# Optimization experiments

Hardware: AMD Instinct MI355X
Metric: run time of the kernel (lower is better)

Reference implementation:

```python
import jax, jax.numpy as jnp
import numpy as np

N_NODES = 100000
N_EDGES = 1600000
N_CRYS = 2000
NODE_F = 64
EDGE_F = 41
N_CONV = 3
H_F = 128
EPS = 1e-5


def _seg_mean(v, idx, n):
    s = jax.ops.segment_sum(v, idx, num_segments=n)
    c = jax.ops.segment_sum(jnp.ones((v.shape[0], 1), v.dtype), idx, num_segments=n)
    return s / jnp.maximum(c, 1.0)


def _bn(x, g, b):
    # training-mode batch norm over dim 0, biased variance (torch semantics)
    m = x.mean(axis=0)
    v = x.var(axis=0)
    return (x - m) * jax.lax.rsqrt(v + EPS) * g + b


def setup_inputs() -> dict:
    key = jax.random.key(0)
    ks = jax.random.split(key, 16)
    inp = {}
    inp['node_fea'] = jax.random.randint(ks[0], (N_NODES,), 0, 101)
    inp['edge_fea'] = jax.random.normal(ks[1], (N_EDGES, EDGE_F), dtype=jnp.float32)
    inp['idx1'] = jax.random.randint(ks[2], (N_EDGES,), 0, N_NODES)
    inp['idx2'] = jax.random.randint(ks[3], (N_EDGES,), 0, N_NODES)
    inp['idx3'] = jnp.sort(jax.random.randint(ks[4], (N_NODES,), 0, N_CRYS))
    # parameters
    din = 2 * NODE_F + EDGE_F
    sc = 1.0 / np.sqrt(din)
    inp['emb'] = jax.random.normal(ks[5], (101, NODE_F), dtype=jnp.float32)
    inp['Wf'] = jax.random.uniform(ks[6], (N_CONV, din, 2 * NODE_F), jnp.float32, -sc, sc)
    inp['bf'] = jax.random.uniform(ks[7], (N_CONV, 2 * NODE_F), jnp.float32, -sc, sc)
    inp['g1'] = jnp.ones((N_CONV, 2 * NODE_F), jnp.float32)
    inp['be1'] = jnp.zeros((N_CONV, 2 * NODE_F), jnp.float32)
    inp['g2'] = jnp.ones((N_CONV, NODE_F), jnp.float32)
    inp['be2'] = jnp.zeros((N_CONV, NODE_F), jnp.float32)
    sc2 = 1.0 / np.sqrt(NODE_F)
    inp['Wc'] = jax.random.uniform(ks[8], (NODE_F, H_F), jnp.float32, -sc2, sc2)
    inp['bc'] = jax.random.uniform(ks[9], (H_F,), jnp.float32, -sc2, sc2)
    sc3 = 1.0 / np.sqrt(H_F)
    inp['Wo'] = jax.random.uniform(ks[10], (H_F, 2), jnp.float32, -sc3, sc3)
    inp['bo'] = jax.random.uniform(ks[11], (2,), jnp.float32, -sc3, sc3)
    return inp


def reference(node_fea, edge_fea, idx1, idx2, idx3, emb, Wf, bf, g1, be1, g2, be2, Wc, bc, Wo, bo):
    x = emb[node_fea]                                   # [N, 64]
    for l in range(N_CONV):
        z12 = jnp.concatenate([x[idx1], x[idx2], edge_fea], axis=1)   # [E, 169]
        z12 = _bn(z12 @ Wf[l] + bf[l], g1[l], be1[l])   # [E, 128]
        gate, conv = jnp.split(z12, 2, axis=1)
        msg = jax.nn.sigmoid(gate) * jax.nn.softplus(conv)
        node_new = _bn(_seg_mean(msg, idx1, N_NODES), g2[l], be2[l])
        x = jax.nn.softplus(x + node_new)
    crys = _seg_mean(x, idx3, N_CRYS)                   # [C, 64]
    crys = jax.nn.softplus(crys @ Wc + bc)              # [C, 128]
    return crys @ Wo + bo                               # [C, 2]
```

## Files before the change

### kernel.cpp

```cpp
#include <hip/hip_runtime.h>
#include <hip/hip_bf16.h>


#define NN 100000
#define NE 1600000
#define NC 2000
#define KPAD 176
#define EFW 48
#define EPSB 1e-5f
#define NCH 1000
#define CH 100

typedef _Float16 f16;
typedef _Float16 half8 __attribute__((ext_vector_type(8)));
typedef _Float16 half2v __attribute__((ext_vector_type(2)));
typedef float f32x16 __attribute__((ext_vector_type(16)));

__device__ __forceinline__ f32x16 zero16() {
    f32x16 v;
#pragma unroll
    for (int i = 0; i < 16; i++) v[i] = 0.f;
    return v;
}
__device__ __forceinline__ float fsoftplus(float x) {
    return fmaxf(x, 0.f) + __logf(1.f + __expf(-fabsf(x)));
}
__device__ __forceinline__ float fsigmoid(float x) {
    return __fdividef(1.f, 1.f + __expf(-x));
}

__global__ void k_prep_x(const int* __restrict__ nf, const float* __restrict__ emb,
                         float* __restrict__ xf, f16* __restrict__ x16) {
    for (int idx = blockIdx.x * blockDim.x + threadIdx.x; idx < NN * 64;
         idx += gridDim.x * blockDim.x) {
        int n = idx >> 6, k = idx & 63;
        float v = emb[nf[n] * 64 + k];
        xf[idx] = v;
        x16[idx] = (f16)v;
    }
}

__global__ void k_deg(const int* __restrict__ idx1, const int* __restrict__ idx3,
                      int* deg1, float* cnt3) {
    for (int i = blockIdx.x * blockDim.x + threadIdx.x; i < NE;
         i += gridDim.x * blockDim.x) {
        atomicAdd(&deg1[idx1[i]], 1);
        if (i < NN) atomicAdd(&cnt3[idx3[i]], 1.f);
    }
}

__global__ void k_scan_a(const int* __restrict__ deg, int* __restrict__ csum) {
    int t = blockIdx.x * blockDim.x + threadIdx.x;
    if (t < NCH) {
        int s = 0;
        int base = t * CH;
        for (int i = 0; i < CH; i++) s += deg[base + i];
        csum[t] = s;
    }
}
__global__ void k_scan_b(const int* __restrict__ csum, int* __restrict__ coff) {
    __shared__ int sc[256];
    int t = threadIdx.x;
    int v[4];
    int part = 0;
#pragma unroll
    for (int q = 0; q < 4; q++) {
        int idx = 4 * t + q;
        v[q] = (idx < NCH) ? csum[idx] : 0;
        part += v[q];
    }
    sc[t] = part;
    __syncthreads();
    for (int off = 1; off < 256; off <<= 1) {
        int add = (t >= off) ? sc[t - off] : 0;
        __syncthreads();
        sc[t] += add;
        __syncthreads();
    }
    int run = sc[t] - part;
#pragma unroll
    for (int q = 0; q < 4; q++) {
        int idx = 4 * t + q;
        if (idx < NCH) coff[idx] = run;
        run += v[q];
    }
}
__global__ void k_scan_c(const int* __restrict__ deg, const int* __restrict__ coff,
                         int* __restrict__ rp) {
    int t = blockIdx.x * blockDim.x + threadIdx.x;
    if (t < NCH) {
        int running = coff[t];
        int base = t * CH;
        for (int i = 0; i < CH; i++) {
            rp[base + i] = running;
            running += deg[base + i];
        }
    }
}

__global__ void k_scatter(const int* __restrict__ idx1, const int* __restrict__ idx2,
                          const int* __restrict__ rp1, int* cur1, int* elist1,
                          int* i1r, int* i2r) {
    for (int e = blockIdx.x * blockDim.x + threadIdx.x; e < NE;
         e += gridDim.x * blockDim.x) {
        int n1 = idx1[e];
        int p = rp1[n1] + atomicAdd(&cur1[n1], 1);
        elist1[p] = e;
        i1r[p] = n1;
        i2r[p] = idx2[e];
    }
}

__global__ void k_prep_efg(const float* __restrict__ ef, const int* __restrict__ elist1,
                           f16* __restrict__ ef16p) {
    for (long idx = (long)blockIdx.x * blockDim.x + threadIdx.x; idx < (long)NE * EFW;
         idx += (long)gridDim.x * blockDim.x) {
        long p = idx / EFW;
        int k = (int)(idx - p * EFW);
        int e = elist1[p];
        float v = (k < 41) ? ef[(size_t)e * 41 + k] : 0.f;
        ef16p[idx] = (f16)v;
    }
}

__global__ void k_wt(const float* __restrict__ Wf_l, f16* __restrict__ WTp) {
    for (int idx = blockIdx.x * blockDim.x + threadIdx.x; idx < 128 * KPAD;
         idx += gridDim.x * blockDim.x) {
        int sl = idx / KPAD, k = idx % KPAD;
        int q = sl >> 5, cl = sl & 31;
        int col = (cl & 16) ? 64 + q * 16 + (cl & 15) : q * 16 + cl;
        float v = (k < 169) ? Wf_l[k * 128 + col] : 0.f;
        WTp[idx] = (f16)v;
    }
}

__global__ __launch_bounds__(256) void k_edge_a(
    const f16* __restrict__ x16, const f16* __restrict__ ef16p,
    const f16* __restrict__ WTp, const int* __restrict__ i1r,
    const int* __restrict__ i2r, float* __restrict__ estats,
    f16* __restrict__ zph) {
    __shared__ float lst[256];
    int tid = threadIdx.x;
    int lane = tid & 63;
    int q = tid >> 6;
    int c = lane & 31, kg = lane >> 5;
    int slot = 32 * q + c;
    int jz = (c & 16) ? 64 + q * 16 + (c & 15) : q * 16 + c;

    half8 bfr[11];
    {
        const f16* bp = WTp + slot * KPAD + kg * 8;
#pragma unroll
        for (int s = 0; s < 11; s++)
            bfr[s] = *reinterpret_cast<const half8*>(bp + s * 16);
    }
    const size_t zoff = 2 * (size_t)(q * 16 + (c & 15)) + ((c >> 4) & 1);

    float s1 = 0.f, s2 = 0.f;
    const int NT = NE / 32;
    for (int tile = blockIdx.x; tile < NT; tile += gridDim.x) {
        int p0 = tile * 32;
        long p = p0 + c;
        int i1 = i1r[p], i2 = i2r[p];
        f32x16 acc = zero16();
#pragma unroll
        for (int s = 0; s < 4; s++) {
            half8 a = *reinterpret_cast<const half8*>(x16 + (size_t)i1 * 64 + s * 16 + kg * 8);
            acc = __builtin_amdgcn_mfma_f32_32x32x16_f16(a, bfr[s], acc, 0, 0, 0);
        }
#pragma unroll
        for (int s = 0; s < 4; s++) {
            half8 a = *reinterpret_cast<const half8*>(x16 + (size_t)i2 * 64 + s * 16 + kg * 8);
            acc = __builtin_amdgcn_mfma_f32_32x32x16_f16(a, bfr[4 + s], acc, 0, 0, 0);
        }
#pragma unroll
        for (int s = 0; s < 3; s++) {
            half8 a = *reinterpret_cast<const half8*>(ef16p + p * EFW + s * 16 + kg * 8);
            acc = __builtin_amdgcn_mfma_f32_32x32x16_f16(a, bfr[8 + s], acc, 0, 0, 0);
        }
#pragma unroll
        for (int r = 0; r < 16; r++) {
            float v = acc[r];
            s1 += v;
            s2 += v * v;
            int row = (r & 3) + 8 * (r >> 2) + 4 * kg;
            zph[(size_t)(p0 + row) * 128 + zoff] = (f16)v;
        }
    }
    s1 += __shfl_xor(s1, 32, 64);
    s2 += __shfl_xor(s2, 32, 64);
    if (kg == 0) {
        lst[jz] = s1;
        lst[128 + jz] = s2;
    }
    __syncthreads();
    atomicAdd(&estats[tid], lst[tid]);
}

__global__ __launch_bounds__(256) void k_nodered(
    const half2v* __restrict__ zp, const int* __restrict__ rp1,
    const int* __restrict__ deg1, const float* __restrict__ estats,
    const float* __restrict__ g1, const float* __restrict__ be1,
    float* __restrict__ raw_out, float* __restrict__ nstats) {
    __shared__ float sstat[128];
    int tid = threadIdx.x;
    int j = tid & 63, wv = tid >> 6;
    if (tid < 128) sstat[tid] = 0.f;
    __syncthreads();
    float mg = estats[j] * (1.f / NE);
    float vg = estats[128 + j] * (1.f / NE) - mg * mg;
    float ag = g1[j] * rsqrtf(vg + EPSB);
    float bg = be1[j] - mg * ag;
    float mc = estats[64 + j] * (1.f / NE);
    float vc = estats[192 + j] * (1.f / NE) - mc * mc;
    float ac = g1[64 + j] * rsqrtf(vc + EPSB);
    float bc = be1[64 + j] - mc * ac;
    float p1 = 0.f, p2 = 0.f;
    for (int n = blockIdx.x * 4 + wv; n < NN; n += gridDim.x * 4) {
        int st = rp1[n], d = deg1[n];
        float acc = 0.f;
#pragma unroll 4
        for (int q = 0; q < d; q++) {
            half2v z = __builtin_nontemporal_load(&zp[(size_t)(st + q) * 64 + j]);
            float g = fsigmoid((float)z[0] * ag + bg);
            float s = fsoftplus((float)z[1] * ac + bc);
            acc += g * s;
        }
        float raw = acc / fmaxf((float)d, 1.f);
        raw_out[(size_t)n * 64 + j] = raw;
        p1 += raw;
        p2 += raw * raw;
    }
    atomicAdd(&sstat[j], p1);
    atomicAdd(&sstat[64 + j], p2);
    __syncthreads();
    if (tid < 128) atomicAdd(&nstats[tid], sstat[tid]);
}

template <bool LAST>
__global__ __launch_bounds__(256) void k_node_apply(
    const float* __restrict__ raw_in, const float* __restrict__ nstats,
    const float* __restrict__ g2, const float* __restrict__ be2,
    float* __restrict__ xf, f16* __restrict__ x16, const int* __restrict__ idx3,
    float* __restrict__ crsum) {
    for (int idx = blockIdx.x * blockDim.x + threadIdx.x; idx < NN * 64;
         idx += gridDim.x * blockDim.x) {
        int n = idx >> 6, j = idx & 63;
        float m = nstats[j] * (1.f / NN);
        float var = nstats[64 + j] * (1.f / NN) - m * m;
        float rs = rsqrtf(var + EPSB);
        float a = g2[j] * rs;
        float b = be2[j] - m * a;
        float v = fsoftplus(xf[idx] + raw_in[idx] * a + b);
        if (LAST) {
            atomicAdd(&crsum[(size_t)idx3[n] * 64 + j], v);
        } else {
            xf[idx] = v;
            x16[idx] = (f16)v;
        }
    }
}

__global__ __launch_bounds__(128) void k_out(const float* __restrict__ crsum,
                                             const float* __restrict__ cnt3,
                                             const float* __restrict__ Wc,
                                             const float* __restrict__ bcv,
                                             const float* __restrict__ Wo,
                                             const float* __restrict__ bo,
                                             float* __restrict__ out) {
    __shared__ float crym[64];
    __shared__ float red[4];
    int c = blockIdx.x, tid = threadIdx.x;
    if (tid < 64) crym[tid] = crsum[c * 64 + tid] / fmaxf(cnt3[c], 1.f);
    __syncthreads();
    float hv = bcv[tid];
#pragma unroll
    for (int k = 0; k < 64; k++) hv += crym[k] * Wc[k * 128 + tid];
    hv = fsoftplus(hv);
    float o0 = hv * Wo[tid * 2 + 0];
    float o1 = hv * Wo[tid * 2 + 1];
#pragma unroll
    for (int off = 32; off > 0; off >>= 1) {
        o0 += __shfl_down(o0, off, 64);
        o1 += __shfl_down(o1, off, 64);
    }
    int wv = tid >> 6;
    if ((tid & 63) == 0) { red[wv * 2] = o0; red[wv * 2 + 1] = o1; }
    __syncthreads();
    if (tid == 0) {
        out[c * 2 + 0] = red[0] + red[2] + bo[0];
        out[c * 2 + 1] = red[1] + red[3] + bo[1];
    }
}

static inline size_t al256(size_t x) { return (x + 255) & ~(size_t)255; }

extern "C" void kernel_launch(void* const* d_in, const int* in_sizes, int n_in,
                              void* d_out, int out_size, void* d_ws, size_t ws_size,
                              hipStream_t stream) {
    const int* node_fea = (const int*)d_in[0];
    const float* edge_fea = (const float*)d_in[1];
    const int* idx1 = (const int*)d_in[2];
    const int* idx2 = (const int*)d_in[3];
    const int* idx3 = (const int*)d_in[4];
    const float* emb = (const float*)d_in[5];
    const float* Wf = (const float*)d_in[6];
    const float* g1 = (const float*)d_in[8];
    const float* be1 = (const float*)d_in[9];
    const float* g2 = (const float*)d_in[10];
    const float* be2 = (const float*)d_in[11];
    const float* Wc = (const float*)d_in[12];
    const float* bc = (const float*)d_in[13];
    const float* Wo = (const float*)d_in[14];
    const float* bo = (const float*)d_in[15];
    float* out = (float*)d_out;
    unsigned char* ws = (unsigned char*)d_ws;

    size_t off = 0;
    size_t o_xf = off;     off = al256(off + (size_t)NN * 64 * 4);
    size_t o_x16 = off;    off = al256(off + (size_t)NN * 64 * 2);
    size_t o_efp = off;    off = al256(off + (size_t)NE * EFW * 2);
    size_t o_WT = off;     off = al256(off + (size_t)128 * KPAD * 2);
    size_t o_rp1 = off;    off = al256(off + (size_t)NN * 4);
    size_t o_el1 = off;    off = al256(off + (size_t)NE * 4);
    size_t o_i1r = off;    off = al256(off + (size_t)NE * 4);
    size_t o_i2r = off;    off = al256(off + (size_t)NE * 4);
    size_t o_raw = off;    off = al256(off + (size_t)NN * 64 * 4);
    size_t o_deg1 = off;   off = al256(off + (size_t)NN * 4);
    size_t o_cur1 = off;   off = al256(off + (size_t)NN * 4);
    size_t o_cnt3 = off;   off = al256(off + (size_t)NC * 4);
    size_t o_csum = off;   off = al256(off + 1024 * 4);
    size_t o_coff = off;   off = al256(off + 1024 * 4);
    size_t o_crsum = off;  off = al256(off + (size_t)NC * 64 * 4);
    size_t prep_zero_end = off;
    size_t o_estats = off; off = al256(off + 256 * 4);
    size_t o_nstats = off; off = al256(off + 128 * 4);
    size_t layer_zero_end = off;
    size_t o_z = off;      off = al256(off + (size_t)NE * 64 * 4);
    (void)ws_size;

    float* xf = (float*)(ws + o_xf);
    f16* x16 = (f16*)(ws + o_x16);
    f16* ef16p = (f16*)(ws + o_efp);
    f16* WTp = (f16*)(ws + o_WT);
    int* rp1 = (int*)(ws + o_rp1);
    int* elist1 = (int*)(ws + o_el1);
    int* i1r = (int*)(ws + o_i1r);
    int* i2r = (int*)(ws + o_i2r);
    float* raw = (float*)(ws + o_raw);
    int* deg1 = (int*)(ws + o_deg1);
    int* cur1 = (int*)(ws + o_cur1);
    float* cnt3 = (float*)(ws + o_cnt3);
    int* csum = (int*)(ws + o_csum);
    int* coff = (int*)(ws + o_coff);
    float* crsum = (float*)(ws + o_crsum);
    float* estats = (float*)(ws + o_estats);
    float* nstats = (float*)(ws + o_nstats);
    f16* zph = (f16*)(ws + o_z);
    half2v* zp = (half2v*)(ws + o_z);

    hipMemsetAsync(ws + o_deg1, 0, prep_zero_end - o_deg1, stream);
    k_prep_x<<<1024, 256, 0, stream>>>(node_fea, emb, xf, x16);
    k_deg<<<2048, 256, 0, stream>>>(idx1, idx3, deg1, cnt3);
    k_scan_a<<<4, 256, 0, stream>>>(deg1, csum);
    k_scan_b<<<1, 256, 0, stream>>>(csum, coff);
    k_scan_c<<<4, 256, 0, stream>>>(deg1, coff, rp1);
    k_scatter<<<2048, 256, 0, stream>>>(idx1, idx2, rp1, cur1, elist1, i1r, i2r);
    k_prep_efg<<<4096, 256, 0, stream>>>(edge_fea, elist1, ef16p);

    for (int l = 0; l < 3; l++) {
        const float* Wf_l = Wf + (size_t)l * 169 * 128;
        hipMemsetAsync(ws + o_estats, 0, layer_zero_end - o_estats, stream);
        k_wt<<<88, 256, 0, stream>>>(Wf_l, WTp);
        k_edge_a<<<4096, 256, 0, stream>>>(x16, ef16p, WTp, i1r, i2r, estats, zph);
        k_nodered<<<4096, 256, 0, stream>>>(zp, rp1, deg1, estats, g1 + l * 128,
                                            be1 + l * 128, raw, nstats);
        if (l < 2) {
            k_node_apply<false><<<1024, 256, 0, stream>>>(raw, nstats, g2 + l * 64,
                                                          be2 + l * 64, xf, x16,
                                                          idx3, crsum);
        } else {
            k_node_apply<true><<<1024, 256, 0, stream>>>(raw, nstats, g2 + l * 64,
                                                         be2 + l * 64, xf, x16,
                                                         idx3, crsum);
        }
    }
    k_out<<<2000, 128, 0, stream>>>(crsum, cnt3, Wc, bc, Wo, bo, out);
}
```

Before: 1.865 ms.

## Prefetch next tile's x[idx2] gather into double-buffered LDS shared across waves

In the edge GEMM kernel, each of the four waves previously gathered the full x[idx2] rows redundantly. Now each wave gathers one 16-column slice into a double-buffered shared-memory tile, and the gather for the next tile is issued before the current tile's MFMAs. This cuts redundant global gathers and hides their latency. In exchange it adds a __syncthreads per tile and extra LDS traffic. The x[idx1] gathers are still done per wave.

```diff
diff --git a/kernel.cpp b/kernel.cpp
--- a/kernel.cpp
+++ b/kernel.cpp
@@ -140,6 +140,7 @@
     const int* __restrict__ i2r, float* __restrict__ estats,
     f16* __restrict__ zph) {
     __shared__ float lst[256];
+    __shared__ f16 abuf[2][4][2][32][8];
     int tid = threadIdx.x;
     int lane = tid & 63;
     int q = tid >> 6;
@@ -158,19 +159,35 @@
 
     float s1 = 0.f, s2 = 0.f;
     const int NT = NE / 32;
-    for (int tile = blockIdx.x; tile < NT; tile += gridDim.x) {
-        int p0 = tile * 32;
+    const int stride = gridDim.x;
+    int t = blockIdx.x;
+    int i1v = i1r[(size_t)t * 32 + c];
+    int i2v = i2r[(size_t)t * 32 + c];
+    *reinterpret_cast<half8*>(&abuf[0][q][kg][c][0]) =
+        *reinterpret_cast<const half8*>(x16 + (size_t)i2v * 64 + q * 16 + kg * 8);
+    __syncthreads();
+    int cur = 0;
+    for (; t < NT; t += stride) {
+        int tn = t + stride;
+        bool hasn = (tn < NT);
+        int i1n = 0, i2n = 0;
+        half8 gn;
+        if (hasn) {
+            i1n = i1r[(size_t)tn * 32 + c];
+            i2n = i2r[(size_t)tn * 32 + c];
+            gn = *reinterpret_cast<const half8*>(x16 + (size_t)i2n * 64 + q * 16 + kg * 8);
+        }
+        int p0 = t * 32;
         long p = p0 + c;
-        int i1 = i1r[p], i2 = i2r[p];
         f32x16 acc = zero16();
 #pragma unroll
         for (int s = 0; s < 4; s++) {
-            half8 a = *reinterpret_cast<const half8*>(x16 + (size_t)i1 * 64 + s * 16 + kg * 8);
+            half8 a = *reinterpret_cast<const half8*>(x16 + (size_t)i1v * 64 + s * 16 + kg * 8);
             acc = __builtin_amdgcn_mfma_f32_32x32x16_f16(a, bfr[s], acc, 0, 0, 0);
         }
 #pragma unroll
         for (int s = 0; s < 4; s++) {
-            half8 a = *reinterpret_cast<const half8*>(x16 + (size_t)i2 * 64 + s * 16 + kg * 8);
+            half8 a = *reinterpret_cast<const half8*>(&abuf[cur][s][kg][c][0]);
             acc = __builtin_amdgcn_mfma_f32_32x32x16_f16(a, bfr[4 + s], acc, 0, 0, 0);
         }
 #pragma unroll
@@ -186,6 +203,13 @@
             int row = (r & 3) + 8 * (r >> 2) + 4 * kg;
             zph[(size_t)(p0 + row) * 128 + zoff] = (f16)v;
         }
+        if (hasn) {
+            *reinterpret_cast<half8*>(&abuf[cur ^ 1][q][kg][c][0]) = gn;
+            i1v = i1n;
+            i2v = i2n;
+        }
+        __syncthreads();
+        cur ^= 1;
     }
     s1 += __shfl_xor(s1, 32, 64);
     s2 += __shfl_xor(s2, 32, 64);
```

New measurement: 1.828 ms. 1.02x faster.

## Restructure edge GEMM: per-wave tiles, LDS weights, prefetched gathers

Applied to the files above, without the earlier changes.

Each wave now owns a whole 32-edge tile and computes all four 32-column output groups, reading the weight fragments from LDS. Before, each of the four waves gathered the same node rows for its own column group, so this removes that 4x redundant gather traffic. The next tile's indices and features are prefetched into registers (software pipelining), and streaming loads and stores use nontemporal hints. The cost is higher register pressure from the double-buffered A fragments and the per-group stats, plus LDS reads of B on every MFMA. The grid size is halved.

```diff
diff --git a/kernel.cpp b/kernel.cpp
--- a/kernel.cpp
+++ b/kernel.cpp
@@ -6,6 +6,7 @@
 #define NE 1600000
 #define NC 2000
 #define KPAD 176
+#define NFRAG 11
 #define EFW 48
 #define EPSB 1e-5f
 #define NCH 1000
@@ -127,8 +128,8 @@
     for (int idx = blockIdx.x * blockDim.x + threadIdx.x; idx < 128 * KPAD;
          idx += gridDim.x * blockDim.x) {
         int sl = idx / KPAD, k = idx % KPAD;
-        int q = sl >> 5, cl = sl & 31;
-        int col = (cl & 16) ? 64 + q * 16 + (cl & 15) : q * 16 + cl;
+        int g = sl >> 5, cl = sl & 31;
+        int col = (cl & 16) ? 64 + g * 16 + (cl & 15) : g * 16 + cl;
         float v = (k < 169) ? Wf_l[k * 128 + col] : 0.f;
         WTp[idx] = (f16)v;
     }
@@ -139,59 +140,112 @@
     const f16* __restrict__ WTp, const int* __restrict__ i1r,
     const int* __restrict__ i2r, float* __restrict__ estats,
     f16* __restrict__ zph) {
+    __shared__ f16 ldsB[NFRAG][128][16];
     __shared__ float lst[256];
     int tid = threadIdx.x;
+    for (int i = tid; i < NFRAG * 128 * 2; i += 256) {
+        int s = i >> 8, rem = i & 255;
+        int slot = rem >> 1, half = rem & 1;
+        *reinterpret_cast<half8*>(&ldsB[s][slot][half * 8]) =
+            *reinterpret_cast<const half8*>(WTp + slot * KPAD + s * 16 + half * 8);
+    }
+    lst[tid] = 0.f;
+    __syncthreads();
+
     int lane = tid & 63;
-    int q = tid >> 6;
     int c = lane & 31, kg = lane >> 5;
-    int slot = 32 * q + c;
-    int jz = (c & 16) ? 64 + q * 16 + (c & 15) : q * 16 + c;
-
-    half8 bfr[11];
+    const int zbase = 2 * (c & 15) + ((c >> 4) & 1);
+    const int ldso = c * 32 + kg * 16;
+
+    float s1[4] = {0.f, 0.f, 0.f, 0.f}, s2[4] = {0.f, 0.f, 0.f, 0.f};
+
+    const int NT = NE / 32;
+    const int wstride = gridDim.x * 4;
+    int t = blockIdx.x * 4 + (tid >> 6);
+
+    half8 a[NFRAG];
     {
-        const f16* bp = WTp + slot * KPAD + kg * 8;
-#pragma unroll
-        for (int s = 0; s < 11; s++)
-            bfr[s] = *reinterpret_cast<const half8*>(bp + s * 16);
-    }
-    const size_t zoff = 2 * (size_t)(q * 16 + (c & 15)) + ((c >> 4) & 1);
-
-    float s1 = 0.f, s2 = 0.f;
-    const int NT = NE / 32;
-    for (int tile = blockIdx.x; tile < NT; tile += gridDim.x) {
-        int p0 = tile * 32;
-        long p = p0 + c;
-        int i1 = i1r[p], i2 = i2r[p];
-        f32x16 acc = zero16();
-#pragma unroll
-        for (int s = 0; s < 4; s++) {
-            half8 a = *reinterpret_cast<const half8*>(x16 + (size_t)i1 * 64 + s * 16 + kg * 8);
-            acc = __builtin_amdgcn_mfma_f32_32x32x16_f16(a, bfr[s], acc, 0, 0, 0);
-        }
-#pragma unroll
-        for (int s = 0; s < 4; s++) {
-            half8 a = *reinterpret_cast<const half8*>(x16 + (size_t)i2 * 64 + s * 16 + kg * 8);
-            acc = __builtin_amdgcn_mfma_f32_32x32x16_f16(a, bfr[4 + s], acc, 0, 0, 0);
-        }
-#pragma unroll
-        for (int s = 0; s < 3; s++) {
-            half8 a = *reinterpret_cast<const half8*>(ef16p + p * EFW + s * 16 + kg * 8);
-            acc = __builtin_amdgcn_mfma_f32_32x32x16_f16(a, bfr[8 + s], acc, 0, 0, 0);
-        }
-#pragma unroll
-        for (int r = 0; r < 16; r++) {
-            float v = acc[r];
-            s1 += v;
-            s2 += v * v;
-            int row = (r & 3) + 8 * (r >> 2) + 4 * kg;
-            zph[(size_t)(p0 + row) * 128 + zoff] = (f16)v;
-        }
-    }
-    s1 += __shfl_xor(s1, 32, 64);
-    s2 += __shfl_xor(s2, 32, 64);
+        size_t pb = (size_t)t * 32 + c;
+        int i1v = i1r[pb], i2v = i2r[pb];
+#pragma unroll
+        for (int s = 0; s < 4; s++)
+            a[s] = *reinterpret_cast<const half8*>(x16 + (size_t)i1v * 64 + s * 16 + kg * 8);
+#pragma unroll
+        for (int s = 0; s < 4; s++)
+            a[4 + s] = *reinterpret_cast<const half8*>(x16 + (size_t)i2v * 64 + s * 16 + kg * 8);
+#pragma unroll
+        for (int s = 0; s < 3; s++)
+            a[8 + s] = __builtin_nontemporal_load(
+                reinterpret_cast<const half8*>(ef16p + pb * EFW + s * 16 + kg * 8));
+    }
+    int tn = t + wstride;
+    int i1n = 0, i2n = 0;
+    if (tn < NT) {
+        i1n = i1r[(size_t)tn * 32 + c];
+        i2n = i2r[(size_t)tn * 32 + c];
+    }
+
+    while (true) {
+        bool hasn = (tn < NT);
+        half8 nx[NFRAG];
+        int i1nn = 0, i2nn = 0;
+        if (hasn) {
+#pragma unroll
+            for (int s = 0; s < 4; s++)
+                nx[s] = *reinterpret_cast<const half8*>(x16 + (size_t)i1n * 64 + s * 16 + kg * 8);
+#pragma unroll
+            for (int s = 0; s < 4; s++)
+                nx[4 + s] = *reinterpret_cast<const half8*>(x16 + (size_t)i2n * 64 + s * 16 + kg * 8);
+#pragma unroll
+            for (int s = 0; s < 3; s++)
+                nx[8 + s] = __builtin_nontemporal_load(reinterpret_cast<const half8*>(
+                    ef16p + ((size_t)tn * 32 + c) * EFW + s * 16 + kg * 8));
+            int tnn = tn + wstride;
+            if (tnn < NT) {
+                i1nn = i1r[(size_t)tnn * 32 + c];
+                i2nn = i2r[(size_t)tnn * 32 + c];
+            }
+        }
+        int p0 = t * 32;
+#pragma unroll
+        for (int g = 0; g < 4; g++) {
+            f32x16 acc = zero16();
+#pragma unroll
+            for (int s = 0; s < NFRAG; s++) {
+                half8 b = *reinterpret_cast<const half8*>(
+                    reinterpret_cast<const char*>(&ldsB[0][0][0]) + s * 4096 + g * 1024 + ldso);
+                acc = __builtin_amdgcn_mfma_f32_32x32x16_f16(a[s], b, acc, 0, 0, 0);
+            }
+#pragma unroll
+            for (int r = 0; r < 16; r++) {
+                float v = acc[r];
+                s1[g] += v;
+                s2[g] += v * v;
+                int row = (r & 3) + 8 * (r >> 2) + 4 * kg;
+                __builtin_nontemporal_store(
+                    (f16)v, zph + (size_t)(p0 + row) * 128 + 32 * g + zbase);
+            }
+        }
+        if (!hasn) break;
+        t = tn;
+        tn += wstride;
+#pragma unroll
+        for (int s = 0; s < NFRAG; s++) a[s] = nx[s];
+        i1n = i1nn;
+        i2n = i2nn;
+    }
+#pragma unroll
+    for (int g = 0; g < 4; g++) {
+        s1[g] += __shfl_xor(s1[g], 32, 64);
+        s2[g] += __shfl_xor(s2[g], 32, 64);
+    }
     if (kg == 0) {
-        lst[jz] = s1;
-        lst[128 + jz] = s2;
+#pragma unroll
+        for (int g = 0; g < 4; g++) {
+            int jz = (c & 16) ? 64 + g * 16 + (c & 15) : g * 16 + c;
+            atomicAdd(&lst[jz], s1[g]);
+            atomicAdd(&lst[128 + jz], s2[g]);
+        }
     }
     __syncthreads();
     atomicAdd(&estats[tid], lst[tid]);
@@ -372,7 +426,7 @@
         const float* Wf_l = Wf + (size_t)l * 169 * 128;
         hipMemsetAsync(ws + o_estats, 0, layer_zero_end - o_estats, stream);
         k_wt<<<88, 256, 0, stream>>>(Wf_l, WTp);
-        k_edge_a<<<4096, 256, 0, stream>>>(x16, ef16p, WTp, i1r, i2r, estats, zph);
+        k_edge_a<<<2048, 256, 0, stream>>>(x16, ef16p, WTp, i1r, i2r, estats, zph);
         k_nodered<<<4096, 256, 0, stream>>>(zp, rp1, deg1, estats, g1 + l * 128,
                                             be1 + l * 128, raw, nstats);
         if (l < 2) {
```

Result: faster. 1.755 ms (-5.9%).
